# Optimization experiments

Hardware: AMD Instinct MI355X
Metric: run time of the kernel (lower is better)

The kernel has to match this reference:

```python
import jax, jax.numpy as jnp
import numpy as np

B, T, I, H = 16384, 10, 184, 128


def _lstm_dir(x, w_ih, w_hh, b_ih, b_hh, reverse):
    # x: (B, T, I); PyTorch gate order: i, f, g, o
    h0 = jnp.zeros((x.shape[0], H), x.dtype)
    c0 = jnp.zeros((x.shape[0], H), x.dtype)
    xs = jnp.swapaxes(x, 0, 1)  # (T, B, I)
    if reverse:
        xs = xs[::-1]
    # precompute input projections for all timesteps: (T, B, 4H)
    xproj = jnp.einsum('tbi,gi->tbg', xs, w_ih) + b_ih + b_hh

    def step(carry, xp):
        h, c = carry
        gates = xp + h @ w_hh.T
        i, f, g, o = jnp.split(gates, 4, axis=-1)
        i = jax.nn.sigmoid(i); f = jax.nn.sigmoid(f)
        g = jnp.tanh(g); o = jax.nn.sigmoid(o)
        c = f * c + i * g
        h = o * jnp.tanh(c)
        return (h, c), h

    _, hs = jax.lax.scan(step, (h0, c0), xproj)  # (T, B, H)
    if reverse:
        hs = hs[::-1]
    return jnp.swapaxes(hs, 0, 1)  # (B, T, H)


def _bilstm(x, wf, whf, bf, bhf, wb, whb, bb, bhb):
    fwd = _lstm_dir(x, wf, whf, bf, bhf, False)
    bwd = _lstm_dir(x, wb, whb, bb, bhb, True)
    return jnp.concatenate([fwd, bwd], axis=-1)  # (B, T, 2H)


def setup_inputs() -> dict:
    key = jax.random.key(0)
    ks = jax.random.split(key, 21)
    s = 0.05
    d = {"x": jax.random.normal(ks[0], (B, T, I), jnp.float32)}
    def p(k, shape):
        return jax.random.normal(k, shape, jnp.float32) * s
    # rnn1: input 184 -> hidden 128, bidirectional
    d["w_ih1_f"] = p(ks[1], (4 * H, I));   d["w_hh1_f"] = p(ks[2], (4 * H, H))
    d["b_ih1_f"] = p(ks[3], (4 * H,));     d["b_hh1_f"] = p(ks[4], (4 * H,))
    d["w_ih1_b"] = p(ks[5], (4 * H, I));   d["w_hh1_b"] = p(ks[6], (4 * H, H))
    d["b_ih1_b"] = p(ks[7], (4 * H,));     d["b_hh1_b"] = p(ks[8], (4 * H,))
    # rnn2: input 256 -> hidden 128, bidirectional
    d["w_ih2_f"] = p(ks[9], (4 * H, 2 * H));  d["w_hh2_f"] = p(ks[10], (4 * H, H))
    d["b_ih2_f"] = p(ks[11], (4 * H,));       d["b_hh2_f"] = p(ks[12], (4 * H,))
    d["w_ih2_b"] = p(ks[13], (4 * H, 2 * H)); d["w_hh2_b"] = p(ks[14], (4 * H, H))
    d["b_ih2_b"] = p(ks[15], (4 * H,));       d["b_hh2_b"] = p(ks[16], (4 * H,))
    # head: Linear(512,64) -> relu -> Linear(64,1)
    d["fc1_w"] = p(ks[17], (64, 512)); d["fc1_b"] = p(ks[18], (64,))
    d["fc2_w"] = p(ks[19], (1, 64));   d["fc2_b"] = p(ks[20], (1,))
    return d


def reference(x, w_ih1_f, w_hh1_f, b_ih1_f, b_hh1_f, w_ih1_b, w_hh1_b, b_ih1_b, b_hh1_b,
              w_ih2_f, w_hh2_f, b_ih2_f, b_hh2_f, w_ih2_b, w_hh2_b, b_ih2_b, b_hh2_b,
              fc1_w, fc1_b, fc2_w, fc2_b):
    ot = x.reshape(x.shape[0], x.shape[1], -1)  # (B, T, 184)
    ot = _bilstm(ot, w_ih1_f, w_hh1_f, b_ih1_f, b_hh1_f, w_ih1_b, w_hh1_b, b_ih1_b, b_hh1_b)
    ot = _bilstm(ot, w_ih2_f, w_hh2_f, b_ih2_f, b_hh2_f, w_ih2_b, w_hh2_b, b_ih2_b, b_hh2_b)
    # permute (B, C=256, T) then MaxPool1d(kernel=5, stride=5): windows over time
    Bn = ot.shape[0]
    pooled = jnp.max(ot.reshape(Bn, T // 5, 5, 2 * H), axis=2)  # (B, 2, 256)
    pooled = jnp.transpose(pooled, (0, 2, 1)).reshape(Bn, -1)   # (B, 512) channel-major like torch
    h = jax.nn.relu(pooled @ fc1_w.T + fc1_b)
    return h @ fc2_w.T + fc2_b  # (B, 1)
```

## Files before the change

### kernel.cpp

```cpp
#include <hip/hip_runtime.h>

typedef _Float16 half8_t __attribute__((ext_vector_type(8)));
typedef _Float16 half4_t __attribute__((ext_vector_type(4)));
typedef _Float16 half2_t __attribute__((ext_vector_type(2)));
typedef float floatx4 __attribute__((ext_vector_type(4)));
typedef float float4_t __attribute__((ext_vector_type(4)));
typedef unsigned int uint4_t __attribute__((ext_vector_type(4)));

__device__ __forceinline__ float sigm_f(float v) {
  return __builtin_amdgcn_rcpf(1.f + __expf(-v));
}
__device__ __forceinline__ float tanh_f(float v) {
  return 2.f * __builtin_amdgcn_rcpf(1.f + __expf(-2.f * v)) - 1.f;
}

__device__ __forceinline__ void gl_lds16(const _Float16* g, _Float16* l) {
  __builtin_amdgcn_global_load_lds(
      (const __attribute__((address_space(1))) void*)g,
      (__attribute__((address_space(3))) void*)l, 16, 0, 0);
}

__global__ void prep_kernel(
    const float* __restrict__ wih1f, const float* __restrict__ whh1f,
    const float* __restrict__ bih1f, const float* __restrict__ bhh1f,
    const float* __restrict__ wih1b, const float* __restrict__ whh1b,
    const float* __restrict__ bih1b, const float* __restrict__ bhh1b,
    const float* __restrict__ wih2f, const float* __restrict__ whh2f,
    const float* __restrict__ bih2f, const float* __restrict__ bhh2f,
    const float* __restrict__ wih2b, const float* __restrict__ whh2b,
    const float* __restrict__ bih2b, const float* __restrict__ bhh2b,
    const float* __restrict__ fc1w,
    _Float16* __restrict__ wswz1, _Float16* __restrict__ wswz2,
    _Float16* __restrict__ wfc, float* __restrict__ biasc) {
  const int N1 = 327680, N2 = 393216, NF = 32768, NB = 2048;
  int idx = blockIdx.x * 256 + threadIdx.x;
  if (idx < N1) {
    int d = idx / 163840;
    int r = idx - d * 163840;
    int j = r & 7, lane = (r >> 3) & 63, ntg = (r >> 9) & 31, kt = r >> 14;
    int k = kt * 32 + (lane >> 4) * 8 + j;
    int n = ntg * 16 + (lane & 15);
    int oc = ((n >> 4) & 3) * 128 + (n >> 6) * 16 + (n & 15);
    const float* wih = d ? wih1b : wih1f;
    const float* whh = d ? whh1b : whh1f;
    float v = (k < 184) ? wih[oc * 184 + k]
                        : ((k < 192) ? 0.f : whh[oc * 128 + (k - 192)]);
    wswz1[idx] = (_Float16)v;
  } else if (idx < N1 + N2) {
    int r0 = idx - N1;
    int d = r0 / 196608;
    int r = r0 - d * 196608;
    int j = r & 7, lane = (r >> 3) & 63, ntg = (r >> 9) & 31, kt = r >> 14;
    int k = kt * 32 + (lane >> 4) * 8 + j;
    int n = ntg * 16 + (lane & 15);
    int oc = ((n >> 4) & 3) * 128 + (n >> 6) * 16 + (n & 15);
    const float* wih = d ? wih2b : wih2f;
    const float* whh = d ? whh2b : whh2f;
    float v = (k < 256) ? wih[oc * 256 + k] : whh[oc * 128 + (k - 256)];
    wswz2[r0] = (_Float16)v;
  } else if (idx < N1 + N2 + NF) {
    int r = idx - (N1 + N2);
    int j = r & 7, lane = (r >> 3) & 63, ntg = (r >> 9) & 3, kt = r >> 11;
    int k = kt * 32 + (lane >> 4) * 8 + j;
    int n = ntg * 16 + (lane & 15);
    wfc[r] = (_Float16)fc1w[n * 512 + k];
  } else if (idx < N1 + N2 + NF + NB) {
    int r = idx - (N1 + N2 + NF);
    int n = r & 511, d = (r >> 9) & 1, l = r >> 10;
    int oc = ((n >> 4) & 3) * 128 + (n >> 6) * 16 + (n & 15);
    const float* bi = l ? (d ? bih2b : bih2f) : (d ? bih1b : bih1f);
    const float* bh = l ? (d ? bhh2b : bhh2f) : (d ? bhh1b : bhh1f);
    biasc[r] = bi[oc] + bh[oc];
  }
}

template <int LAYER>
__global__ __launch_bounds__(512, 2) void lstm_kernel(
    const void* __restrict__ xin_v, const _Float16* __restrict__ wswz,
    const float* __restrict__ biasc, _Float16* __restrict__ outp) {
  constexpr int XT = (LAYER == 1) ? 6 : 8;
  constexpr int KT = XT + 4;
  constexpr int RKT = (LAYER == 1) ? 8 : 9;
  constexpr int LKT = KT - RKT;
  constexpr int XHALF = XT * 1024;

  __shared__ __align__(16) _Float16 Xbuf[2 * XHALF];
  __shared__ __align__(16) _Float16 Hbuf[4096];
  __shared__ __align__(16) _Float16 Wlds[LKT * 16384];

  const int tid = threadIdx.x;
  const int cs = tid >> 6;
  const int lane = tid & 63;
  const int q = lane >> 4;
  const int l15 = lane & 15;
  const int lane8 = lane * 8;
  const int dir = blockIdx.y;
  const int row0 = blockIdx.x << 5;
  const int rt0 = blockIdx.x << 1;

  const _Float16* __restrict__ wd = wswz + (size_t)dir * (KT * 16384);
  const float* __restrict__ bd = biasc + (dir << 9);

  float bias_frag[4];
#pragma unroll
  for (int nt = 0; nt < 4; ++nt) bias_frag[nt] = bd[(cs << 6) + (nt << 4) + l15];

  half8_t Wreg[RKT][4];
#pragma unroll
  for (int i = 0; i < RKT; ++i) {
    const _Float16* p = wd + (((size_t)i * 32 + (cs << 2)) * 64 + lane) * 8;
#pragma unroll
    for (int nt = 0; nt < 4; ++nt) Wreg[i][nt] = *(const half8_t*)(p + nt * 512);
  }
#pragma unroll
  for (int it = 0; it < LKT * 4; ++it) {
    int u = tid + it * 512;
    gl_lds16(wd + (size_t)RKT * 16384 + u * 8, Wlds + u * 8);
  }

  float4_t xs[3];
  auto l1_load = [&](int te) {
#pragma unroll
    for (int it = 0; it < 3; ++it) {
      int u = tid + it * 512;
      if (u < 1472) {
        int r = u / 46, c = u - r * 46;
        xs[it] = __builtin_nontemporal_load(
            (const float4_t*)((const float*)xin_v + (size_t)(row0 + r) * 1840 +
                              te * 184 + (c << 2)));
      }
    }
  };
  auto l1_write = [&](int buf) {
    _Float16* xb = Xbuf + buf * XHALF;
#pragma unroll
    for (int it = 0; it < 3; ++it) {
      int u = tid + it * 512;
      if (u < 1472) {
        int r = u / 46, c = u - r * 46, k0 = c << 2;
        half4_t hv;
        hv[0] = (_Float16)xs[it][0]; hv[1] = (_Float16)xs[it][1];
        hv[2] = (_Float16)xs[it][2]; hv[3] = (_Float16)xs[it][3];
        *(half4_t*)(xb + ((k0 >> 5) * 2 + (r >> 4)) * 512 +
                    ((k0 & 31) >> 3) * 128 + (r & 15) * 8 + (k0 & 7)) = hv;
      }
    }
  };
  auto l2_stage = [&](int buf, int te) {
    const _Float16* xf = (const _Float16*)xin_v;
    _Float16* xb = Xbuf + buf * XHALF;
#pragma unroll
    for (int it = 0; it < 2; ++it) {
      int u = tid + it * 512;
      int kt = u >> 7, mt = (u >> 6) & 1, v = u & 63;
      gl_lds16(xf + ((size_t)((rt0 + mt) * 10 + te) * 8 + kt) * 512 + v * 8,
               xb + u * 8);
    }
  };

  {
    uint4_t z = {0u, 0u, 0u, 0u};
    *(uint4_t*)(Hbuf + tid * 8) = z;
    if (LAYER == 1 && tid < 64) {
      half8_t hz;
#pragma unroll
      for (int j = 0; j < 8; ++j) hz[j] = (_Float16)0.f;
      int buf = tid >> 5, r = tid & 31;
      *(half8_t*)(Xbuf + buf * XHALF + (10 + (r >> 4)) * 512 + 384 + (r & 15) * 8) = hz;
    }
  }

  const int te0 = dir ? 9 : 0;
  if (LAYER == 1) { l1_load(te0); l1_write(0); } else { l2_stage(0, te0); }

  float c_state[2][4];
#pragma unroll
  for (int mt = 0; mt < 2; ++mt)
#pragma unroll
    for (int rg = 0; rg < 4; ++rg) c_state[mt][rg] = 0.f;

  float gmax[2][2][4];
  if (LAYER == 2) {
#pragma unroll
    for (int g = 0; g < 2; ++g)
#pragma unroll
      for (int mt = 0; mt < 2; ++mt)
#pragma unroll
        for (int rg = 0; rg < 4; ++rg) gmax[g][mt][rg] = -1e30f;
  }

  __syncthreads();

  for (int t = 0; t < 10; ++t) {
    const int te = dir ? (9 - t) : t;
    const int cur = t & 1;

    if (t < 9) {
      const int ten = dir ? (8 - t) : (t + 1);
      if (LAYER == 1) l1_load(ten);
      else l2_stage(cur ^ 1, ten);
    }

    floatx4 acc[2][4];
#pragma unroll
    for (int mt = 0; mt < 2; ++mt)
#pragma unroll
      for (int nt = 0; nt < 4; ++nt) {
        floatx4 b4 = {bias_frag[nt], bias_frag[nt], bias_frag[nt], bias_frag[nt]};
        acc[mt][nt] = b4;
      }

    const _Float16* xc = Xbuf + cur * XHALF;
#pragma unroll
    for (int i = 0; i < KT; ++i) {
      half8_t bl[4];
      if (i < RKT) {
#pragma unroll
        for (int nt = 0; nt < 4; ++nt) bl[nt] = Wreg[i][nt];
      } else {
#pragma unroll
        for (int nt = 0; nt < 4; ++nt)
          bl[nt] = *(const half8_t*)(Wlds + (i - RKT) * 16384 +
                                     (((cs << 2) + nt) * 64 + lane) * 8);
      }
      const _Float16* abase =
          (i < XT) ? (xc + i * 1024 + lane8) : (Hbuf + (i - XT) * 1024 + lane8);
#pragma unroll
      for (int mt = 0; mt < 2; ++mt) {
        half8_t a = *(const half8_t*)(abase + mt * 512);
#pragma unroll
        for (int nt = 0; nt < 4; ++nt)
          acc[mt][nt] = __builtin_amdgcn_mfma_f32_16x16x32_f16(a, bl[nt], acc[mt][nt], 0, 0, 0);
      }
    }

    if (LAYER == 1 && t > 0) {
      const int t_prev = dir ? (10 - t) : (t - 1);
      int u = tid, hk = u >> 7, mt = (u >> 6) & 1, v = u & 63;
      __builtin_nontemporal_store(
          *(const uint4_t*)(Hbuf + u * 8),
          (uint4_t*)(outp + (((size_t)(rt0 + mt) * 10 + t_prev) * 8 + (dir << 2) + hk) * 512 +
                     v * 8));
    }
    if (LAYER == 1 && t < 9) l1_write(cur ^ 1);

    __syncthreads();

#pragma unroll
    for (int mt = 0; mt < 2; ++mt) {
#pragma unroll
      for (int rg = 0; rg < 4; ++rg) {
        float ig = sigm_f(acc[mt][0][rg]);
        float fg = sigm_f(acc[mt][1][rg]);
        float gg = tanh_f(acc[mt][2][rg]);
        float og = sigm_f(acc[mt][3][rg]);
        float c = fg * c_state[mt][rg] + ig * gg;
        c_state[mt][rg] = c;
        float h = og * tanh_f(c);
        if (LAYER == 2) {
          int g = (te < 5) ? 0 : 1;
          gmax[g][mt][rg] = fmaxf(gmax[g][mt][rg], h);
        }
        Hbuf[((cs >> 1) * 2 + mt) * 512 + (((cs & 1) * 2) + (l15 >> 3)) * 128 +
             ((q << 2) + rg) * 8 + (l15 & 7)] = (_Float16)h;
      }
    }
    __syncthreads();
  }

  if (LAYER == 1) {
    const int t_last = dir ? 0 : 9;
    int u = tid, hk = u >> 7, mt = (u >> 6) & 1, v = u & 63;
    __builtin_nontemporal_store(
        *(const uint4_t*)(Hbuf + u * 8),
        (uint4_t*)(outp + (((size_t)(rt0 + mt) * 10 + t_last) * 8 + (dir << 2) + hk) * 512 +
                   v * 8));
  } else {
    _Float16* P = Xbuf;
#pragma unroll
    for (int mt = 0; mt < 2; ++mt)
#pragma unroll
      for (int rg = 0; rg < 4; ++rg)
#pragma unroll
        for (int g = 0; g < 2; ++g)
          P[(mt * 16 + (q << 2) + rg) * 256 + ((cs << 4) + l15) * 2 + g] =
              (_Float16)gmax[g][mt][rg];
    __syncthreads();
#pragma unroll
    for (int it = 0; it < 2; ++it) {
      int u = tid + it * 512;
      int r = u >> 5, v = u & 31;
      __builtin_nontemporal_store(
          *(const uint4_t*)(P + u * 8),
          (uint4_t*)(outp + (size_t)(row0 + r) * 512 + (dir << 8) + v * 8));
    }
  }
}

__global__ __launch_bounds__(256) void fc_kernel(
    const _Float16* __restrict__ pooled_g, const _Float16* __restrict__ wfc,
    const float* __restrict__ fc1b, const float* __restrict__ fc2w,
    const float* __restrict__ fc2b, float* __restrict__ out) {
  __shared__ __align__(16) _Float16 pooled[64 * 520];
  const int tid = threadIdx.x;
  const int s0 = blockIdx.x << 6;

#pragma unroll
  for (int it = 0; it < 16; ++it) {
    int u = tid + it * 256;
    int s = u >> 6, v = u & 63;
    *(uint4_t*)(pooled + s * 520 + v * 8) =
        *(const uint4_t*)(pooled_g + (size_t)(s0 + s) * 512 + v * 8);
  }
  __syncthreads();

  const int wid = tid >> 6, lane = tid & 63, q = lane >> 4, l15 = lane & 15;
  const int m0 = wid << 4;

  const floatx4 fzero = {0.f, 0.f, 0.f, 0.f};
  floatx4 acc[4];
#pragma unroll
  for (int nt = 0; nt < 4; ++nt) acc[nt] = fzero;

#pragma unroll
  for (int kt = 0; kt < 16; ++kt) {
    half8_t a = *(const half8_t*)(pooled + (m0 + l15) * 520 + (kt << 5) + (q << 3));
#pragma unroll
    for (int nt = 0; nt < 4; ++nt) {
      half8_t b = *(const half8_t*)(wfc + ((((size_t)kt << 2) + nt) * 64 + lane) * 8);
      acc[nt] = __builtin_amdgcn_mfma_f32_16x16x32_f16(a, b, acc[nt], 0, 0, 0);
    }
  }

  float b1[4], w2[4];
#pragma unroll
  for (int nt = 0; nt < 4; ++nt) {
    b1[nt] = fc1b[(nt << 4) + l15];
    w2[nt] = fc2w[(nt << 4) + l15];
  }
  const float c2b = fc2b[0];

#pragma unroll
  for (int rg = 0; rg < 4; ++rg) {
    float v = 0.f;
#pragma unroll
    for (int nt = 0; nt < 4; ++nt)
      v += fmaxf(acc[nt][rg] + b1[nt], 0.f) * w2[nt];
    v += __shfl_xor(v, 1, 64);
    v += __shfl_xor(v, 2, 64);
    v += __shfl_xor(v, 4, 64);
    v += __shfl_xor(v, 8, 64);
    if (l15 == 0) out[s0 + m0 + (q << 2) + rg] = v + c2b;
  }
}

extern "C" void kernel_launch(void* const* d_in, const int* in_sizes, int n_in,
                              void* d_out, int out_size, void* d_ws, size_t ws_size,
                              hipStream_t stream) {
  const float* x     = (const float*)d_in[0];
  const float* wih1f = (const float*)d_in[1];
  const float* whh1f = (const float*)d_in[2];
  const float* bih1f = (const float*)d_in[3];
  const float* bhh1f = (const float*)d_in[4];
  const float* wih1b = (const float*)d_in[5];
  const float* whh1b = (const float*)d_in[6];
  const float* bih1b = (const float*)d_in[7];
  const float* bhh1b = (const float*)d_in[8];
  const float* wih2f = (const float*)d_in[9];
  const float* whh2f = (const float*)d_in[10];
  const float* bih2f = (const float*)d_in[11];
  const float* bhh2f = (const float*)d_in[12];
  const float* wih2b = (const float*)d_in[13];
  const float* whh2b = (const float*)d_in[14];
  const float* bih2b = (const float*)d_in[15];
  const float* bhh2b = (const float*)d_in[16];
  const float* fc1w  = (const float*)d_in[17];
  const float* fc1b  = (const float*)d_in[18];
  const float* fc2w  = (const float*)d_in[19];
  const float* fc2b  = (const float*)d_in[20];
  float* out = (float*)d_out;

  if (ws_size < (size_t)169287680) return;
  _Float16* pooled_g = (_Float16*)d_ws;
  _Float16* h1out = pooled_g + (size_t)8388608;
  _Float16* wswz1 = h1out + (size_t)41943040;
  _Float16* wswz2 = wswz1 + 327680;
  _Float16* wfc   = wswz2 + 393216;
  float* biasc    = (float*)(wfc + 32768);

  prep_kernel<<<2952, 256, 0, stream>>>(
      wih1f, whh1f, bih1f, bhh1f, wih1b, whh1b, bih1b, bhh1b,
      wih2f, whh2f, bih2f, bhh2f, wih2b, whh2b, bih2b, bhh2b, fc1w,
      wswz1, wswz2, wfc, biasc);
  lstm_kernel<1><<<dim3(512, 2), 512, 0, stream>>>(x, wswz1, biasc, h1out);
  lstm_kernel<2><<<dim3(512, 2), 512, 0, stream>>>(h1out, wswz2, biasc + 1024, pooled_g);
  fc_kernel<<<256, 256, 0, stream>>>(pooled_g, wfc, fc1b, fc2w, fc2b, out);
}
```

Measured before the change: 554.8 us.

## Software-pipeline input projection ahead of recurrence with double-buffered hidden state

Restructures the LSTM timestep loop so the input-projection MFMAs for step t+1 are computed right after the gate activations of step t, leaving only the hidden-state GEMM on the serial path. The hidden-state buffer is doubled so reads and writes alternate, which removes one __syncthreads per step, and input staging now prefetches two steps ahead. The cost is extra LDS, a second set of accumulator registers that may add pressure under the 512x2 launch bounds, and more complex buffer indexing.

```diff
diff --git a/kernel.cpp b/kernel.cpp
--- a/kernel.cpp
+++ b/kernel.cpp
@@ -85,7 +85,7 @@
   constexpr int XHALF = XT * 1024;
 
   __shared__ __align__(16) _Float16 Xbuf[2 * XHALF];
-  __shared__ __align__(16) _Float16 Hbuf[4096];
+  __shared__ __align__(16) _Float16 Hbuf[2 * 4096];
   __shared__ __align__(16) _Float16 Wlds[LKT * 16384];
 
   const int tid = threadIdx.x;
@@ -158,6 +158,41 @@
     }
   };
 
+  auto bfrag = [&](int kt, half8_t* bl) {
+    if (kt < RKT) {
+#pragma unroll
+      for (int nt = 0; nt < 4; ++nt) bl[nt] = Wreg[kt][nt];
+    } else {
+#pragma unroll
+      for (int nt = 0; nt < 4; ++nt)
+        bl[nt] = *(const half8_t*)(Wlds + (kt - RKT) * 16384 +
+                                   (((cs << 2) + nt) * 64 + lane) * 8);
+    }
+  };
+  auto xgemm = [&](const _Float16* xb, floatx4 (*ac)[4]) {
+#pragma unroll
+    for (int i = 0; i < XT; ++i) {
+      half8_t bl[4];
+      bfrag(i, bl);
+#pragma unroll
+      for (int mt = 0; mt < 2; ++mt) {
+        half8_t a = *(const half8_t*)(xb + i * 1024 + mt * 512 + lane8);
+#pragma unroll
+        for (int nt = 0; nt < 4; ++nt)
+          ac[mt][nt] = __builtin_amdgcn_mfma_f32_16x16x32_f16(a, bl[nt], ac[mt][nt], 0, 0, 0);
+      }
+    }
+  };
+  auto accinit = [&](floatx4 (*ac)[4]) {
+#pragma unroll
+    for (int mt = 0; mt < 2; ++mt)
+#pragma unroll
+      for (int nt = 0; nt < 4; ++nt) {
+        floatx4 b4 = {bias_frag[nt], bias_frag[nt], bias_frag[nt], bias_frag[nt]};
+        ac[mt][nt] = b4;
+      }
+  };
+
   {
     uint4_t z = {0u, 0u, 0u, 0u};
     *(uint4_t*)(Hbuf + tid * 8) = z;
@@ -171,7 +206,14 @@
   }
 
   const int te0 = dir ? 9 : 0;
-  if (LAYER == 1) { l1_load(te0); l1_write(0); } else { l2_stage(0, te0); }
+  const int te1 = dir ? 8 : 1;
+  if (LAYER == 1) {
+    l1_load(te0); l1_write(0);
+    l1_load(te1); l1_write(1);
+  } else {
+    l2_stage(0, te0);
+    l2_stage(1, te1);
+  }
 
   float c_state[2][4];
 #pragma unroll
@@ -191,61 +233,45 @@
 
   __syncthreads();
 
+  floatx4 acc[2][4];
+  accinit(acc);
+  xgemm(Xbuf, acc);
+  __syncthreads();
+
   for (int t = 0; t < 10; ++t) {
+    const int cur = t & 1;
     const int te = dir ? (9 - t) : t;
-    const int cur = t & 1;
-
-    if (t < 9) {
-      const int ten = dir ? (8 - t) : (t + 1);
-      if (LAYER == 1) l1_load(ten);
-      else l2_stage(cur ^ 1, ten);
-    }
-
-    floatx4 acc[2][4];
-#pragma unroll
-    for (int mt = 0; mt < 2; ++mt)
-#pragma unroll
-      for (int nt = 0; nt < 4; ++nt) {
-        floatx4 b4 = {bias_frag[nt], bias_frag[nt], bias_frag[nt], bias_frag[nt]};
-        acc[mt][nt] = b4;
-      }
-
-    const _Float16* xc = Xbuf + cur * XHALF;
-#pragma unroll
-    for (int i = 0; i < KT; ++i) {
-      half8_t bl[4];
-      if (i < RKT) {
-#pragma unroll
-        for (int nt = 0; nt < 4; ++nt) bl[nt] = Wreg[i][nt];
-      } else {
-#pragma unroll
-        for (int nt = 0; nt < 4; ++nt)
-          bl[nt] = *(const half8_t*)(Wlds + (i - RKT) * 16384 +
-                                     (((cs << 2) + nt) * 64 + lane) * 8);
-      }
-      const _Float16* abase =
-          (i < XT) ? (xc + i * 1024 + lane8) : (Hbuf + (i - XT) * 1024 + lane8);
-#pragma unroll
-      for (int mt = 0; mt < 2; ++mt) {
-        half8_t a = *(const half8_t*)(abase + mt * 512);
-#pragma unroll
-        for (int nt = 0; nt < 4; ++nt)
-          acc[mt][nt] = __builtin_amdgcn_mfma_f32_16x16x32_f16(a, bl[nt], acc[mt][nt], 0, 0, 0);
-      }
+
+    if (t < 8) {
+      const int te2 = dir ? (7 - t) : (t + 2);
+      if (LAYER == 1) l1_load(te2);
+      else l2_stage(cur, te2);
     }
 
     if (LAYER == 1 && t > 0) {
       const int t_prev = dir ? (10 - t) : (t - 1);
       int u = tid, hk = u >> 7, mt = (u >> 6) & 1, v = u & 63;
       __builtin_nontemporal_store(
-          *(const uint4_t*)(Hbuf + u * 8),
+          *(const uint4_t*)(Hbuf + cur * 4096 + u * 8),
           (uint4_t*)(outp + (((size_t)(rt0 + mt) * 10 + t_prev) * 8 + (dir << 2) + hk) * 512 +
                      v * 8));
     }
-    if (LAYER == 1 && t < 9) l1_write(cur ^ 1);
-
-    __syncthreads();
-
+
+    const _Float16* hb = Hbuf + cur * 4096;
+#pragma unroll
+    for (int i = 0; i < 4; ++i) {
+      half8_t bl[4];
+      bfrag(XT + i, bl);
+#pragma unroll
+      for (int mt = 0; mt < 2; ++mt) {
+        half8_t a = *(const half8_t*)(hb + i * 1024 + mt * 512 + lane8);
+#pragma unroll
+        for (int nt = 0; nt < 4; ++nt)
+          acc[mt][nt] = __builtin_amdgcn_mfma_f32_16x16x32_f16(a, bl[nt], acc[mt][nt], 0, 0, 0);
+      }
+    }
+
+    _Float16* hw = Hbuf + (cur ^ 1) * 4096;
 #pragma unroll
     for (int mt = 0; mt < 2; ++mt) {
 #pragma unroll
@@ -261,10 +287,23 @@
           int g = (te < 5) ? 0 : 1;
           gmax[g][mt][rg] = fmaxf(gmax[g][mt][rg], h);
         }
-        Hbuf[((cs >> 1) * 2 + mt) * 512 + (((cs & 1) * 2) + (l15 >> 3)) * 128 +
-             ((q << 2) + rg) * 8 + (l15 & 7)] = (_Float16)h;
-      }
-    }
+        hw[((cs >> 1) * 2 + mt) * 512 + (((cs & 1) * 2) + (l15 >> 3)) * 128 +
+           ((q << 2) + rg) * 8 + (l15 & 7)] = (_Float16)h;
+      }
+    }
+
+    if (LAYER == 1 && t < 8) l1_write(cur);
+
+    if (t < 9) {
+      floatx4 accN[2][4];
+      accinit(accN);
+      xgemm(Xbuf + (cur ^ 1) * XHALF, accN);
+#pragma unroll
+      for (int mt = 0; mt < 2; ++mt)
+#pragma unroll
+        for (int nt = 0; nt < 4; ++nt) acc[mt][nt] = accN[mt][nt];
+    }
+
     __syncthreads();
   }
 
```

Result: faster. 508.6 us (-8.3%).
